# Performance work log

Measured on AMD Instinct MI355X. Metric: run time of the kernel, lower is better.

## Reference

```python
import jax, jax.numpy as jnp
import numpy as np
from jax import lax

RADIUS = 2
DILATION = 2
KS = 2 * RADIUS + 1  # 5
PERM = np.array([6, 8, 1, 11, 2, 10, 0, 7, 9, 4, 5, 3])


def _shift_kernels():
    # Reproduce the torch index construction in numpy (all constants).
    six = np.array([[0, 1, 1], [1, 1, 0], [1, 0, 1], [1, 1, 2], [2, 1, 1], [1, 2, 1]])
    # pairwise squared distances between the 6 neighbourhood offsets
    d = ((six[:, None, :] - six[None, :, :]) ** 2).sum(-1)
    x, y = np.meshgrid(np.arange(6), np.arange(6), indexing='ij')
    mask = (x > y).reshape(-1) & (d == 2).reshape(-1)
    idx1 = np.repeat(six[:, None, :], 6, axis=1).reshape(-1, 3)[mask]
    idx2 = np.repeat(six[None, :, :], 6, axis=0).reshape(-1, 3)[mask]
    k1 = np.zeros((12, 1, 3, 3, 3), np.float32)
    k2 = np.zeros((12, 1, 3, 3, 3), np.float32)
    r = np.arange(12)
    k1[r, 0, idx1[:, 0], idx1[:, 1], idx1[:, 2]] = 1.0
    k2[r, 0, idx2[:, 0], idx2[:, 1], idx2[:, 2]] = 1.0
    return jnp.asarray(k1), jnp.asarray(k2)

_K1, _K2 = _shift_kernels()
DN = ('NCDHW', 'OIDHW', 'NCDHW')


def _rep_pad(x, p):
    return jnp.pad(x, ((0, 0), (0, 0), (p, p), (p, p), (p, p)), mode='edge')


def mindssc(img):
    # img: [N,1,D,H,W]
    p1 = _rep_pad(img, DILATION)
    c1 = lax.conv_general_dilated(p1, _K1, (1, 1, 1), 'VALID',
                                  rhs_dilation=(DILATION,) * 3, dimension_numbers=DN)
    c2 = lax.conv_general_dilated(p1, _K2, (1, 1, 1), 'VALID',
                                  rhs_dilation=(DILATION,) * 3, dimension_numbers=DN)
    diff2 = (c1 - c2) ** 2  # [N,12,D,H,W]
    p2 = _rep_pad(diff2, RADIUS)
    ssd = lax.reduce_window(p2, 0.0, lax.add, (1, 1, KS, KS, KS),
                            (1, 1, 1, 1, 1), 'VALID') / float(KS ** 3)
    mind = ssd - jnp.min(ssd, axis=1, keepdims=True)
    mind_var = jnp.mean(mind, axis=1, keepdims=True)
    m = jnp.mean(mind_var)
    mind_var = jnp.clip(mind_var, m * 0.001, m * 1000.0)
    mind = jnp.exp(-mind / mind_var)
    return mind[:, PERM]


def setup_inputs() -> dict:
    key = jax.random.key(0)
    k1, k2 = jax.random.split(key)
    shape = (1, 1, 128, 128, 128)
    return {
        'y_true': jax.random.normal(k1, shape, dtype=jnp.float32),
        'y_pred': jax.random.normal(k2, shape, dtype=jnp.float32),
    }


def reference(y_true, y_pred):
    return jnp.mean((mindssc(y_pred) - mindssc(y_true)) ** 2)
```

## Files before the change

kernel.cpp:

```cpp
#include <hip/hip_runtime.h>

#define DIM   128
#define DMASK 127
#define PLANE (DIM * DIM)
#define VOX   (1 << 21)
#define NCH   12

#define CHS   (VOX + 2048)
#define IMGS  (NCH * CHS + 1024)

typedef __attribute__((ext_vector_type(2))) _Float16 half2v;
typedef __attribute__((ext_vector_type(4))) _Float16 half4v;

__constant__ int c_sd1[12] = { 0, 0, 0, 0, 0, 2, 2, 2, 0, 0, 0, 0};
__constant__ int c_sh1[12] = { 0,-2,-2, 0, 0, 0, 0, 0, 2, 2, 2, 2};
__constant__ int c_sw1[12] = {-2, 0, 0, 2, 2, 0, 0, 0, 0, 0, 0, 0};
__constant__ int c_sd2[12] = {-2,-2, 0,-2, 0, 0, 0, 0,-2, 0, 0, 2};
__constant__ int c_sh2[12] = { 0, 0, 0, 0,-2, 0,-2, 0, 0, 0, 0, 0};
__constant__ int c_sw2[12] = { 0, 0,-2, 0, 0,-2, 0, 2, 0,-2, 2, 0};

__device__ __forceinline__ int clamp7(int v) { return min(max(v, 0), DMASK); }

__global__ __launch_bounds__(256, 3) void f123(const float* __restrict__ img0,
                                               const float* __restrict__ img1,
                                               _Float16* __restrict__ Sall) {
    const float* img = blockIdx.y ? img1 : img0;
    _Float16* outS = Sall + (size_t)blockIdx.y * IMGS;
    const char* imgc = (const char*)img;

    int wid = (blockIdx.x << 2) + (threadIdx.x >> 6);
    int ch = wid >> 7;
    int hs = (wid >> 3) & 15;
    int ds = wid & 7;
    int h0 = hs << 3;
    int d0 = ds << 4;
    int l  = threadIdx.x & 63;

    int sd1 = c_sd1[ch], sh1 = c_sh1[ch], sw1 = c_sw1[ch];
    int sd2 = c_sd2[ch], sh2 = c_sh2[ch], sw2 = c_sw2[ch];

    int rowOffA[12], rowOffB[12];
#pragma unroll
    for (int r = 0; r < 12; ++r) {
        int hq = clamp7(h0 - 2 + r);
        rowOffA[r] = clamp7(hq + sh1) * (DIM * 4);
        rowOffB[r] = clamp7(hq + sh2) * (DIM * 4);
    }

    int c2 = l << 1;
    int colA = min(max(c2 + sw1, 0), 126) * 4;
    int colB = min(max(c2 + sw2, 0), 126) * 4;
    bool fixAlo = (sw1 < 0) && (l == 0);
    bool fixAhi = (sw1 > 0) && (l == 63);
    bool fixBlo = (sw2 < 0) && (l == 0);
    bool fixBhi = (sw2 > 0) && (l == 63);

    float2 win[8];
    half2v hist[5][8];
#pragma unroll
    for (int k = 0; k < 8; ++k) {
        win[k].x = 0.0f; win[k].y = 0.0f;
#pragma unroll
        for (int s = 0; s < 5; ++s) hist[s][k] = half2v{(_Float16)0.0f, (_Float16)0.0f};
    }

    _Float16* dstBase = outS + (size_t)ch * CHS + h0 * DIM + c2;

    for (int oo = 0; oo < 4; ++oo) {
#pragma unroll
        for (int s5 = 0; s5 < 5; ++s5) {
            int it = oo * 5 + s5;
            int dp = clamp7(d0 - 2 + it);
            int pOffA = clamp7(dp + sd1) * (PLANE * 4);
            int pOffB = clamp7(dp + sd2) * (PLANE * 4);

            float tX[12], tY[12];
#pragma unroll
            for (int r = 0; r < 12; ++r) {
                float2 a = *(const float2*)(imgc + (pOffA + rowOffA[r] + colA));
                float2 b = *(const float2*)(imgc + (pOffB + rowOffB[r] + colB));
                a.y = fixAlo ? a.x : a.y;  a.x = fixAhi ? a.y : a.x;
                b.y = fixBlo ? b.x : b.y;  b.x = fixBhi ? b.y : b.x;
                float dx = a.x - b.x; dx *= dx;
                float dy = a.y - b.y; dy *= dy;
                float lx = __shfl_up(dx, 1, 64);
                float ly = __shfl_up(dy, 1, 64);
                float rx = __shfl_down(dx, 1, 64);
                float ry = __shfl_down(dy, 1, 64);
                ly = (l == 0)  ? dx : ly;
                rx = (l == 63) ? dy : rx;
                float m = ly + dx + dy + rx;
                tX[r] = lx + m;
                tY[r] = m + ry;
            }

            float sx = tX[0] + tX[1] + tX[2] + tX[3] + tX[4];
            float sy = tY[0] + tY[1] + tY[2] + tY[3] + tY[4];
            bool dowrite = (it >= 4);
            _Float16* dstD = dstBase + (size_t)(d0 + it - 4) * PLANE;
#pragma unroll
            for (int k = 0; k < 8; ++k) {
                half2v hv = { (_Float16)sx, (_Float16)sy };
                half2v old = hist[s5][k];
                win[k].x += (float)hv[0] - (float)old[0];
                win[k].y += (float)hv[1] - (float)old[1];
                hist[s5][k] = hv;
                if (dowrite) {
                    half2v ov = { (_Float16)win[k].x, (_Float16)win[k].y };
                    *(half2v*)(dstD + k * DIM) = ov;
                }
                if (k < 7) {
                    sx += tX[k + 5] - tX[k];
                    sy += tY[k + 5] - tY[k];
                }
            }
        }
    }
}

__global__ __launch_bounds__(256, 3) void kmse(const _Float16* __restrict__ S0,
                                               const _Float16* __restrict__ S1,
                                               float* __restrict__ partial) {
    int t = blockIdx.x * 256 + threadIdx.x;

    half4v v0[NCH], v1[NCH];
#pragma unroll
    for (int ch = 0; ch < NCH; ++ch)
        v0[ch] = ((const half4v*)(S0 + (size_t)ch * CHS))[t];
#pragma unroll
    for (int ch = 0; ch < NCH; ++ch)
        v1[ch] = ((const half4v*)(S1 + (size_t)ch * CHS))[t];

    float mn0[4], sm0[4], mn1[4], sm1[4];
#pragma unroll
    for (int j = 0; j < 4; ++j) {
        mn0[j] = 3.4e38f; sm0[j] = 0.0f;
        mn1[j] = 3.4e38f; sm1[j] = 0.0f;
    }
#pragma unroll
    for (int ch = 0; ch < NCH; ++ch)
#pragma unroll
        for (int j = 0; j < 4; ++j) {
            float s0 = (float)v0[ch][j];
            float s1 = (float)v1[ch][j];
            mn0[j] = fminf(mn0[j], s0); sm0[j] += s0;
            mn1[j] = fminf(mn1[j], s1); sm1[j] += s1;
        }

    float inv0[4], inv1[4];
#pragma unroll
    for (int j = 0; j < 4; ++j) {
        inv0[j] = __fdividef(1.0f, sm0[j] * (1.0f / 12.0f) - mn0[j]);
        inv1[j] = __fdividef(1.0f, sm1[j] * (1.0f / 12.0f) - mn1[j]);
    }

    float acc = 0.0f;
#pragma unroll
    for (int ch = 0; ch < NCH; ++ch)
#pragma unroll
        for (int j = 0; j < 4; ++j) {
            float e0 = __expf(-((float)v0[ch][j] - mn0[j]) * inv0[j]);
            float e1 = __expf(-((float)v1[ch][j] - mn1[j]) * inv1[j]);
            float df = e0 - e1;
            acc += df * df;
        }

#pragma unroll
    for (int off = 32; off > 0; off >>= 1)
        acc += __shfl_down(acc, off, 64);
    __shared__ float smem[4];
    int lane = threadIdx.x & 63, wv = threadIdx.x >> 6;
    if (lane == 0) smem[wv] = acc;
    __syncthreads();
    if (threadIdx.x == 0)
        partial[blockIdx.x] = smem[0] + smem[1] + smem[2] + smem[3];
}

__global__ __launch_bounds__(256) void kred(const float* __restrict__ partial,
                                            float* __restrict__ out) {
    int tid = threadIdx.x;
    float acc = 0.0f;
#pragma unroll
    for (int k = 0; k < 8; ++k)
        acc += partial[tid + (k << 8)];
#pragma unroll
    for (int off = 32; off > 0; off >>= 1)
        acc += __shfl_down(acc, off, 64);
    __shared__ float smem[4];
    int lane = tid & 63, wv = tid >> 6;
    if (lane == 0) smem[wv] = acc;
    __syncthreads();
    if (tid == 0)
        out[0] = (smem[0] + smem[1] + smem[2] + smem[3])
               * (1.0f / (12.0f * (float)VOX));
}

__global__ void kdiag(float* out, float ws_mb) { out[0] = ws_mb; }

extern "C" void kernel_launch(void* const* d_in, const int* in_sizes, int n_in,
                              void* d_out, int out_size, void* d_ws, size_t ws_size,
                              hipStream_t stream) {
    const float* y_true = (const float*)d_in[0];
    const float* y_pred = (const float*)d_in[1];
    float* out = (float*)d_out;

    const size_t NEED = 2ull * IMGS * sizeof(_Float16) + 8192 + 64;
    if (ws_size < NEED) {
        kdiag<<<1, 1, 0, stream>>>(out, (float)(ws_size >> 20));
        return;
    }

    _Float16* S0      = (_Float16*)d_ws;
    _Float16* S1      = S0 + (size_t)IMGS;
    float*    partial = (float*)(S1 + (size_t)IMGS);

    f123<<<dim3(384, 2), 256, 0, stream>>>(y_true, y_pred, S0);
    kmse<<<VOX / 4 / 256, 256, 0, stream>>>(S0, S1, partial);
    kred<<<1, 256, 0, stream>>>(partial, out);
}
```

Measured before the change: 129.6 us.

## Interleave channels per voxel pair, put all channels in one block, use DPP shifts

Measured after the change: 193.2 us. 49.2% more time.

```diff
diff --git a/kernel.cpp b/kernel.cpp
--- a/kernel.cpp
+++ b/kernel.cpp
@@ -6,11 +6,8 @@
 #define VOX   (1 << 21)
 #define NCH   12
 
-#define CHS   (VOX + 2048)
-#define IMGS  (NCH * CHS + 1024)
-
 typedef __attribute__((ext_vector_type(2))) _Float16 half2v;
-typedef __attribute__((ext_vector_type(4))) _Float16 half4v;
+typedef __attribute__((ext_vector_type(8))) _Float16 half8v;
 
 __constant__ int c_sd1[12] = { 0, 0, 0, 0, 0, 2, 2, 2, 0, 0, 0, 0};
 __constant__ int c_sh1[12] = { 0,-2,-2, 0, 0, 0, 0, 0, 2, 2, 2, 2};
@@ -21,20 +18,31 @@
 
 __device__ __forceinline__ int clamp7(int v) { return min(max(v, 0), DMASK); }
 
-__global__ __launch_bounds__(256, 3) void f123(const float* __restrict__ img0,
-                                               const float* __restrict__ img1,
-                                               _Float16* __restrict__ Sall) {
+__device__ __forceinline__ float dpp_shr1(float old_, float src) {
+    return __int_as_float(__builtin_amdgcn_update_dpp(
+        __float_as_int(old_), __float_as_int(src), 0x138, 0xF, 0xF, false));
+}
+__device__ __forceinline__ float dpp_shl1(float old_, float src) {
+    return __int_as_float(__builtin_amdgcn_update_dpp(
+        __float_as_int(old_), __float_as_int(src), 0x130, 0xF, 0xF, false));
+}
+
+
+__global__ __launch_bounds__(768) void f123i(const float* __restrict__ img0,
+                                             const float* __restrict__ img1,
+                                             _Float16* __restrict__ S0,
+                                             _Float16* __restrict__ S1) {
     const float* img = blockIdx.y ? img1 : img0;
-    _Float16* outS = Sall + (size_t)blockIdx.y * IMGS;
+    _Float16* Sout   = blockIdx.y ? S1 : S0;
     const char* imgc = (const char*)img;
 
-    int wid = (blockIdx.x << 2) + (threadIdx.x >> 6);
-    int ch = wid >> 7;
-    int hs = (wid >> 3) & 15;
-    int ds = wid & 7;
-    int h0 = hs << 3;
-    int d0 = ds << 4;
-    int l  = threadIdx.x & 63;
+    int tid = threadIdx.x;
+    int ch  = tid >> 6;
+    int l   = tid & 63;
+
+    int bx = blockIdx.x;
+    int h0 = (bx & 15) << 3;
+    int d0 = (bx >> 4) << 4;
 
     int sd1 = c_sd1[ch], sh1 = c_sh1[ch], sw1 = c_sw1[ch];
     int sd2 = c_sd2[ch], sh2 = c_sh2[ch], sw2 = c_sw2[ch];
@@ -64,7 +72,7 @@
         for (int s = 0; s < 5; ++s) hist[s][k] = half2v{(_Float16)0.0f, (_Float16)0.0f};
     }
 
-    _Float16* dstBase = outS + (size_t)ch * CHS + h0 * DIM + c2;
+    char* dstBase = (char*)Sout + ((size_t)h0 * 64 + l) * 48 + ch * 4;
 
     for (int oo = 0; oo < 4; ++oo) {
 #pragma unroll
@@ -83,12 +91,10 @@
                 b.y = fixBlo ? b.x : b.y;  b.x = fixBhi ? b.y : b.x;
                 float dx = a.x - b.x; dx *= dx;
                 float dy = a.y - b.y; dy *= dy;
-                float lx = __shfl_up(dx, 1, 64);
-                float ly = __shfl_up(dy, 1, 64);
-                float rx = __shfl_down(dx, 1, 64);
-                float ry = __shfl_down(dy, 1, 64);
-                ly = (l == 0)  ? dx : ly;
-                rx = (l == 63) ? dy : rx;
+                float lx = dpp_shr1(dx, dx);
+                float ly = dpp_shr1(dx, dy);
+                float rx = dpp_shl1(dy, dx);
+                float ry = dpp_shl1(dy, dy);
                 float m = ly + dx + dy + rx;
                 tX[r] = lx + m;
                 tY[r] = m + ry;
@@ -97,7 +103,7 @@
             float sx = tX[0] + tX[1] + tX[2] + tX[3] + tX[4];
             float sy = tY[0] + tY[1] + tY[2] + tY[3] + tY[4];
             bool dowrite = (it >= 4);
-            _Float16* dstD = dstBase + (size_t)(d0 + it - 4) * PLANE;
+            char* dstD = dstBase + (size_t)(d0 + it - 4) * (8192 * 48);
 #pragma unroll
             for (int k = 0; k < 8; ++k) {
                 half2v hv = { (_Float16)sx, (_Float16)sy };
@@ -107,60 +113,63 @@
                 hist[s5][k] = hv;
                 if (dowrite) {
                     half2v ov = { (_Float16)win[k].x, (_Float16)win[k].y };
-                    *(half2v*)(dstD + k * DIM) = ov;
+                    *(half2v*)(dstD + k * (64 * 48)) = ov;
                 }
                 if (k < 7) {
                     sx += tX[k + 5] - tX[k];
                     sy += tY[k + 5] - tY[k];
                 }
             }
+            __syncthreads();
         }
     }
 }
 
-__global__ __launch_bounds__(256, 3) void kmse(const _Float16* __restrict__ S0,
-                                               const _Float16* __restrict__ S1,
-                                               float* __restrict__ partial) {
+__global__ __launch_bounds__(256) void kmse(const _Float16* __restrict__ S0,
+                                            const _Float16* __restrict__ S1,
+                                            float* __restrict__ partial) {
     int t = blockIdx.x * 256 + threadIdx.x;
 
-    half4v v0[NCH], v1[NCH];
-#pragma unroll
-    for (int ch = 0; ch < NCH; ++ch)
-        v0[ch] = ((const half4v*)(S0 + (size_t)ch * CHS))[t];
-#pragma unroll
-    for (int ch = 0; ch < NCH; ++ch)
-        v1[ch] = ((const half4v*)(S1 + (size_t)ch * CHS))[t];
-
-    float mn0[4], sm0[4], mn1[4], sm1[4];
-#pragma unroll
-    for (int j = 0; j < 4; ++j) {
-        mn0[j] = 3.4e38f; sm0[j] = 0.0f;
-        mn1[j] = 3.4e38f; sm1[j] = 0.0f;
-    }
-#pragma unroll
-    for (int ch = 0; ch < NCH; ++ch)
-#pragma unroll
-        for (int j = 0; j < 4; ++j) {
-            float s0 = (float)v0[ch][j];
-            float s1 = (float)v1[ch][j];
-            mn0[j] = fminf(mn0[j], s0); sm0[j] += s0;
-            mn1[j] = fminf(mn1[j], s1); sm1[j] += s1;
+    const half8v* q0 = (const half8v*)((const char*)S0 + (size_t)t * 48);
+    const half8v* q1 = (const half8v*)((const char*)S1 + (size_t)t * 48);
+    half8v A0[3], A1[3];
+#pragma unroll
+    for (int c = 0; c < 3; ++c) A0[c] = q0[c];
+#pragma unroll
+    for (int c = 0; c < 3; ++c) A1[c] = q1[c];
+
+    float mn0[2], sm0[2], mn1[2], sm1[2];
+#pragma unroll
+    for (int v = 0; v < 2; ++v) {
+        mn0[v] = 3.4e38f; sm0[v] = 0.0f;
+        mn1[v] = 3.4e38f; sm1[v] = 0.0f;
+    }
+#pragma unroll
+    for (int c = 0; c < NCH; ++c)
+#pragma unroll
+        for (int v = 0; v < 2; ++v) {
+            int e = c * 2 + v;
+            float s0 = (float)A0[e >> 3][e & 7];
+            float s1 = (float)A1[e >> 3][e & 7];
+            mn0[v] = fminf(mn0[v], s0); sm0[v] += s0;
+            mn1[v] = fminf(mn1[v], s1); sm1[v] += s1;
         }
 
-    float inv0[4], inv1[4];
-#pragma unroll
-    for (int j = 0; j < 4; ++j) {
-        inv0[j] = __fdividef(1.0f, sm0[j] * (1.0f / 12.0f) - mn0[j]);
-        inv1[j] = __fdividef(1.0f, sm1[j] * (1.0f / 12.0f) - mn1[j]);
+    float inv0[2], inv1[2];
+#pragma unroll
+    for (int v = 0; v < 2; ++v) {
+        inv0[v] = __fdividef(1.0f, sm0[v] * (1.0f / 12.0f) - mn0[v]);
+        inv1[v] = __fdividef(1.0f, sm1[v] * (1.0f / 12.0f) - mn1[v]);
     }
 
     float acc = 0.0f;
 #pragma unroll
-    for (int ch = 0; ch < NCH; ++ch)
-#pragma unroll
-        for (int j = 0; j < 4; ++j) {
-            float e0 = __expf(-((float)v0[ch][j] - mn0[j]) * inv0[j]);
-            float e1 = __expf(-((float)v1[ch][j] - mn1[j]) * inv1[j]);
+    for (int c = 0; c < NCH; ++c)
+#pragma unroll
+        for (int v = 0; v < 2; ++v) {
+            int e = c * 2 + v;
+            float e0 = __expf(-((float)A0[e >> 3][e & 7] - mn0[v]) * inv0[v]);
+            float e1 = __expf(-((float)A1[e >> 3][e & 7] - mn1[v]) * inv1[v]);
             float df = e0 - e1;
             acc += df * df;
         }
@@ -181,7 +190,7 @@
     int tid = threadIdx.x;
     float acc = 0.0f;
 #pragma unroll
-    for (int k = 0; k < 8; ++k)
+    for (int k = 0; k < 16; ++k)
         acc += partial[tid + (k << 8)];
 #pragma unroll
     for (int off = 32; off > 0; off >>= 1)
@@ -204,17 +213,18 @@
     const float* y_pred = (const float*)d_in[1];
     float* out = (float*)d_out;
 
-    const size_t NEED = 2ull * IMGS * sizeof(_Float16) + 8192 + 64;
+    const size_t SIMG = (size_t)VOX * NCH;
+    const size_t NEED = 2 * SIMG * sizeof(_Float16) + 16384 + 64;
     if (ws_size < NEED) {
         kdiag<<<1, 1, 0, stream>>>(out, (float)(ws_size >> 20));
         return;
     }
 
     _Float16* S0      = (_Float16*)d_ws;
-    _Float16* S1      = S0 + (size_t)IMGS;
-    float*    partial = (float*)(S1 + (size_t)IMGS);
-
-    f123<<<dim3(384, 2), 256, 0, stream>>>(y_true, y_pred, S0);
-    kmse<<<VOX / 4 / 256, 256, 0, stream>>>(S0, S1, partial);
+    _Float16* S1      = S0 + SIMG;
+    float*    partial = (float*)(S1 + SIMG);
+
+    f123i<<<dim3(128, 2), 768, 0, stream>>>(y_true, y_pred, S0, S1);
+    kmse<<<VOX / 2 / 256, 256, 0, stream>>>(S0, S1, partial);
     kred<<<1, 256, 0, stream>>>(partial, out);
 }
```
